# Kernel optimization log

Hardware: AMD Instinct MI355X
Metric: run time of the kernel (lower is better)

Reference implementation:

```python
import jax, jax.numpy as jnp
import numpy as np

B, T, D, H = 4, 2048, 512, 8
DH = D // H

def setup_inputs() -> dict:
    key = jax.random.key(0)
    k1, k2, k3, k4 = jax.random.split(key, 4)
    scale = 1.0 / np.sqrt(D)
    return {
        "x": jax.random.normal(k1, (B, T, D), dtype=jnp.float32),
        "attn_mask": jnp.ones((B, T), dtype=jnp.int32),
        "bias": jax.random.normal(k2, (B, T, T), dtype=jnp.float32),
        "W_qkv": jax.random.normal(k3, (D, 3 * D), dtype=jnp.float32) * scale,
        "W_out": jax.random.normal(k4, (D, D), dtype=jnp.float32) * scale,
    }

def reference(x, attn_mask, bias, W_qkv, W_out):
    qkv = x @ W_qkv                      # [B,T,3D]
    q, k, v = jnp.split(qkv, 3, axis=-1)
    def heads(t):                        # [B,T,D] -> [B,H,T,DH]
        return t.reshape(B, T, H, DH).transpose(0, 2, 1, 3)
    q, k, v = heads(q), heads(k), heads(v)
    logits = jnp.einsum('bhqd,bhkd->bhqk', q, k) / np.sqrt(DH)
    logits = logits + bias[:, None, :, :]
    mask = (attn_mask[:, None, None, :] != 0)
    logits = jnp.where(mask, logits, -jnp.inf)
    attn = jax.nn.softmax(logits, axis=-1)
    out = jnp.einsum('bhqk,bhkd->bhqd', attn, v)  # [B,H,T,DH]
    out = out.transpose(0, 2, 1, 3).reshape(B, T, D)
    return out @ W_out
```

## Files before the change

### kernel.cpp

```cpp
#include <hip/hip_runtime.h>
#include <hip/hip_bf16.h>
#include <stdint.h>

#define Bc 4
#define Tc 2048
#define Dc 512
#define Hc 8

typedef __bf16 bf16x8 __attribute__((ext_vector_type(8)));
typedef float  f32x4  __attribute__((ext_vector_type(4)));
typedef unsigned short u16x8 __attribute__((ext_vector_type(8)));

__device__ __forceinline__ unsigned short f2b(float f) {
  union { float f; unsigned u; } v; v.f = f;
  unsigned r = v.u + 0x7fffu + ((v.u >> 16) & 1u);
  return (unsigned short)(r >> 16);
}

__device__ __forceinline__ bf16x8 ld_frag(const unsigned short* p) {
  u16x8 u = *(const u16x8*)p;
  return __builtin_bit_cast(bf16x8, u);
}

__device__ __forceinline__ void gload_lds16(const unsigned short* g, unsigned short* l) {
  __builtin_amdgcn_global_load_lds((const __attribute__((address_space(1))) void*)g,
                                   (__attribute__((address_space(3))) void*)l,
                                   16, 0, 0);
}

__device__ __forceinline__ unsigned cvtpk_bf16(float lo, float hi) {
  unsigned r;
  asm("v_cvt_pk_bf16_f32 %0, %1, %2" : "=v"(r) : "v"(lo), "v"(hi));
  return r;
}

__global__ __launch_bounds__(256) void cvt_bf16(const float* __restrict__ in,
                                                unsigned short* __restrict__ out, int n) {
  int i = (blockIdx.x * 256 + threadIdx.x) * 8;
  if (i >= n) return;
  float4 a = *(const float4*)&in[i];
  float4 b = *(const float4*)&in[i + 4];
  u16x8 r;
  r[0] = f2b(a.x); r[1] = f2b(a.y); r[2] = f2b(a.z); r[3] = f2b(a.w);
  r[4] = f2b(b.x); r[5] = f2b(b.y); r[6] = f2b(b.z); r[7] = f2b(b.w);
  *(u16x8*)&out[i] = r;
}

__global__ __launch_bounds__(256) void transp_bf16(const float* __restrict__ in,
                                                   unsigned short* __restrict__ out,
                                                   int R, int C) {
  __shared__ float tile[32][33];
  int c0 = blockIdx.x * 32, r0 = blockIdx.y * 32;
  int lx = threadIdx.x & 31, ly = threadIdx.x >> 5;
  #pragma unroll
  for (int i = 0; i < 32; i += 8) tile[ly + i][lx] = in[(size_t)(r0 + ly + i) * C + c0 + lx];
  __syncthreads();
  #pragma unroll
  for (int i = 0; i < 32; i += 8) out[(size_t)(c0 + ly + i) * R + r0 + lx] = f2b(tile[lx][ly + i]);
}

__global__ __launch_bounds__(256) void transp_v(const unsigned short* __restrict__ qkv,
                                                unsigned short* __restrict__ vtg) {
  __shared__ unsigned short tile[32][34];
  int t0 = blockIdx.x * 32;
  int d0 = blockIdx.y * 32;
  int b  = blockIdx.z;
  int lx = threadIdx.x & 31, ly = threadIdx.x >> 5;
  #pragma unroll
  for (int i = 0; i < 32; i += 8)
    tile[ly + i][lx] = qkv[(size_t)(b * Tc + t0 + ly + i) * 1536 + 1024 + d0 + lx];
  __syncthreads();
  #pragma unroll
  for (int i = 0; i < 32; i += 8)
    vtg[(size_t)(b * 512 + d0 + ly + i) * Tc + t0 + lx] = tile[lx][ly + i];
}

template <int N, int OUTF32>
__global__ __launch_bounds__(256) void gemm_bt(const unsigned short* __restrict__ A,
                                               const unsigned short* __restrict__ Bt,
                                               void* __restrict__ Cout, int M, int K) {
  __shared__ unsigned short As[128 * 32];
  __shared__ unsigned short Bs[128 * 32];
  const int tid = threadIdx.x;
  const int lane = tid & 63;
  const int wid = tid >> 6;
  const int wm = (wid >> 1) * 64;
  const int wn = (wid & 1) * 64;
  const int m0 = blockIdx.x * 128;
  const int n0 = blockIdx.y * 128;
  const int l15 = lane & 15;
  const int lg = lane >> 4;

  f32x4 acc[4][4];
  #pragma unroll
  for (int i = 0; i < 4; i++)
    #pragma unroll
    for (int j = 0; j < 4; j++) acc[i][j] = (f32x4){0.f, 0.f, 0.f, 0.f};

  const int srow = tid >> 2;
  const int scol = (tid & 3) * 8;

  for (int k0 = 0; k0 < K; k0 += 32) {
    __syncthreads();
    gload_lds16(&A[(size_t)(m0 + srow) * K + k0 + scol],      &As[tid * 8]);
    gload_lds16(&A[(size_t)(m0 + 64 + srow) * K + k0 + scol], &As[2048 + tid * 8]);
    gload_lds16(&Bt[(size_t)(n0 + srow) * K + k0 + scol],      &Bs[tid * 8]);
    gload_lds16(&Bt[(size_t)(n0 + 64 + srow) * K + k0 + scol], &Bs[2048 + tid * 8]);
    __syncthreads();
    bf16x8 af[4], bfr[4];
    #pragma unroll
    for (int m = 0; m < 4; m++) af[m] = ld_frag(&As[(wm + m * 16 + l15) * 32 + lg * 8]);
    #pragma unroll
    for (int n = 0; n < 4; n++) bfr[n] = ld_frag(&Bs[(wn + n * 16 + l15) * 32 + lg * 8]);
    #pragma unroll
    for (int m = 0; m < 4; m++)
      #pragma unroll
      for (int n = 0; n < 4; n++)
        acc[m][n] = __builtin_amdgcn_mfma_f32_16x16x32_bf16(af[m], bfr[n], acc[m][n], 0, 0, 0);
  }

  #pragma unroll
  for (int m = 0; m < 4; m++)
    #pragma unroll
    for (int n = 0; n < 4; n++)
      #pragma unroll
      for (int j = 0; j < 4; j++) {
        int row = m0 + wm + m * 16 + lg * 4 + j;
        int col = n0 + wn + n * 16 + l15;
        float v = acc[m][n][j];
        if (OUTF32) ((float*)Cout)[(size_t)row * N + col] = v;
        else ((unsigned short*)Cout)[(size_t)row * N + col] = f2b(v);
      }
}

__global__ __launch_bounds__(256) void attn_kernel(const unsigned short* __restrict__ qkv,
                                                   const unsigned short* __restrict__ vtg,
                                                   const float* __restrict__ bias,
                                                   const int* __restrict__ amask,
                                                   unsigned short* __restrict__ ctx) {
  __shared__ unsigned short Ks[64 * 64];
  __shared__ unsigned short Vs[64 * 64];
  __shared__ unsigned short Pt[4][16 * 64];

  const int NQ = Tc / 64;
  const int bid = blockIdx.x;
  const int b = bid / (Hc * NQ);
  const int h = (bid / NQ) % Hc;
  const int q0 = (bid % NQ) * 64;
  const int tid = threadIdx.x;
  const int lane = tid & 63;
  const int w = tid >> 6;
  const int l15 = lane & 15;
  const int lg = lane >> 4;

  const float LOG2E = 1.44269504f;
  const float SC = 0.125f * LOG2E;

  const int qrow = q0 + w * 16 + l15;
  const size_t qoff = (size_t)(b * Tc + qrow) * 1536 + h * 64;
  bf16x8 qf0 = ld_frag(&qkv[qoff + lg * 8]);
  bf16x8 qf1 = ld_frag(&qkv[qoff + 32 + lg * 8]);

  u16x8 ou;
  #pragma unroll
  for (int e = 0; e < 8; e++) ou[e] = 0x3f80;
  const bf16x8 ones = __builtin_bit_cast(bf16x8, ou);

  f32x4 o[4];
  f32x4 osum = (f32x4){0.f, 0.f, 0.f, 0.f};
  #pragma unroll
  for (int n = 0; n < 4; n++) o[n] = (f32x4){0.f, 0.f, 0.f, 0.f};

  const int skey = tid >> 3;
  const int sc = tid & 7;
  const int sgc = sc ^ (skey & 7);

  const size_t kcol = (size_t)b * Tc * 1536 + 512 + h * 64;
  const unsigned short* vrow = &vtg[(size_t)(b * 512 + h * 64) * Tc];

  const float* bq = bias + (size_t)(b * Tc + q0 + w * 16 + l15) * Tc;
  const int* mq = amask + b * Tc;

  unsigned short* ptw = &Pt[w][0];

  for (int kt = 0; kt < Tc; kt += 64) {
    __syncthreads();
    {
      const size_t kbase = kcol + (size_t)kt * 1536;
      gload_lds16(&qkv[kbase + (size_t)skey * 1536 + sgc * 8],        &Ks[tid * 8]);
      gload_lds16(&qkv[kbase + (size_t)(skey + 32) * 1536 + sgc * 8], &Ks[2048 + tid * 8]);
      gload_lds16(&vrow[(size_t)skey * Tc + kt + sgc * 8],        &Vs[tid * 8]);
      gload_lds16(&vrow[(size_t)(skey + 32) * Tc + kt + sgc * 8], &Vs[2048 + tid * 8]);
    }
    float bf_[4][4];
    #pragma unroll
    for (int t2 = 0; t2 < 4; t2++) {
      float4 bb = *(const float4*)&bq[kt + t2 * 16 + lg * 4];
      int4 mm = *(const int4*)&mq[kt + t2 * 16 + lg * 4];
      bf_[t2][0] = mm.x ? bb.x * LOG2E : -1e30f;
      bf_[t2][1] = mm.y ? bb.y * LOG2E : -1e30f;
      bf_[t2][2] = mm.z ? bb.z * LOG2E : -1e30f;
      bf_[t2][3] = mm.w ? bb.w * LOG2E : -1e30f;
    }
    __syncthreads();

    f32x4 s[4];
    __builtin_amdgcn_s_setprio(1);
    #pragma unroll
    for (int t2 = 0; t2 < 4; t2++) {
      int key = t2 * 16 + l15;
      bf16x8 kb0 = ld_frag(&Ks[key * 64 + ((lg) ^ (key & 7)) * 8]);
      bf16x8 kb1 = ld_frag(&Ks[key * 64 + ((4 + lg) ^ (key & 7)) * 8]);
      f32x4 z = (f32x4){0.f, 0.f, 0.f, 0.f};
      z = __builtin_amdgcn_mfma_f32_16x16x32_bf16(kb0, qf0, z, 0, 0, 0);
      z = __builtin_amdgcn_mfma_f32_16x16x32_bf16(kb1, qf1, z, 0, 0, 0);
      s[t2] = z;
    }
    __builtin_amdgcn_s_setprio(0);

    #pragma unroll
    for (int t2 = 0; t2 < 4; t2++) {
      #pragma unroll
      for (int j = 0; j < 4; j++)
        s[t2][j] = exp2f(fmaf(s[t2][j], SC, bf_[t2][j]));
      uint2 pw;
      pw.x = cvtpk_bf16(s[t2][0], s[t2][1]);
      pw.y = cvtpk_bf16(s[t2][2], s[t2][3]);
      const int cp = (2 * t2 + (lg >> 1)) ^ (l15 & 7);
      *(uint2*)&ptw[l15 * 64 + cp * 8 + (lg & 1) * 4] = pw;
    }

    __builtin_amdgcn_s_setprio(1);
    #pragma unroll
    for (int ks = 0; ks < 2; ks++) {
      bf16x8 pa = ld_frag(&ptw[l15 * 64 + ((ks * 4 + lg) ^ (l15 & 7)) * 8]);
      osum = __builtin_amdgcn_mfma_f32_16x16x32_bf16(pa, ones, osum, 0, 0, 0);
      #pragma unroll
      for (int n = 0; n < 4; n++) {
        int d = n * 16 + l15;
        bf16x8 vb = ld_frag(&Vs[d * 64 + ((ks * 4 + lg) ^ (d & 7)) * 8]);
        o[n] = __builtin_amdgcn_mfma_f32_16x16x32_bf16(pa, vb, o[n], 0, 0, 0);
      }
    }
    __builtin_amdgcn_s_setprio(0);
  }

  #pragma unroll
  for (int n = 0; n < 4; n++)
    #pragma unroll
    for (int j = 0; j < 4; j++) {
      int q = q0 + w * 16 + lg * 4 + j;
      ctx[(size_t)(b * Tc + q) * Dc + h * 64 + n * 16 + l15] = f2b(o[n][j] / osum[j]);
    }
}

extern "C" void kernel_launch(void* const* d_in, const int* in_sizes, int n_in,
                              void* d_out, int out_size, void* d_ws, size_t ws_size,
                              hipStream_t stream) {
  const float* x     = (const float*)d_in[0];
  const int*   amask = (const int*)d_in[1];
  const float* bias  = (const float*)d_in[2];
  const float* Wqkv  = (const float*)d_in[3];
  const float* Wout  = (const float*)d_in[4];
  float* out = (float*)d_out;
  char* ws = (char*)d_ws;

  unsigned short* xb    = (unsigned short*)(ws + 0);
  unsigned short* wqkvT = (unsigned short*)(ws + 8388608);
  unsigned short* woutT = (unsigned short*)(ws + 9961472);
  unsigned short* qkv   = (unsigned short*)(ws + 10485760);
  unsigned short* ctx   = (unsigned short*)(ws + 35651584);
  unsigned short* vtg   = (unsigned short*)(ws + 44040192);

  cvt_bf16<<<2048, 256, 0, stream>>>(x, xb, Bc * Tc * Dc);
  transp_bf16<<<dim3(48, 16), 256, 0, stream>>>(Wqkv, wqkvT, 512, 1536);
  transp_bf16<<<dim3(16, 16), 256, 0, stream>>>(Wout, woutT, 512, 512);
  gemm_bt<1536, 0><<<dim3(64, 12), 256, 0, stream>>>(xb, wqkvT, (void*)qkv, 8192, 512);
  transp_v<<<dim3(64, 16, 4), 256, 0, stream>>>(qkv, vtg);
  attn_kernel<<<1024, 256, 0, stream>>>(qkv, vtg, bias, amask, ctx);
  gemm_bt<512, 1><<<dim3(64, 4), 256, 0, stream>>>(ctx, woutT, (void*)out, 8192, 512);
}
```

Measured before the change: 167.4 us.

## Halve attention block to 32 query rows and precompute additive float mask

The attention kernel now runs with 2 waves (32 query rows) per block and 2048 blocks instead of 4 waves and 1024 blocks, so each block's K/V tile loads are spread over 128 threads in four passes. A small pre-kernel converts the int attention mask into an additive float vector (0 or -1e30), and the bias computation becomes a single fma instead of a select. This raises block count and occupancy granularity but doubles K/V tile loading per query row, increasing L2/global traffic for K and V.

```diff
diff --git a/kernel.cpp b/kernel.cpp
--- a/kernel.cpp
+++ b/kernel.cpp
@@ -44,6 +44,12 @@
   r[0] = f2b(a.x); r[1] = f2b(a.y); r[2] = f2b(a.z); r[3] = f2b(a.w);
   r[4] = f2b(b.x); r[5] = f2b(b.y); r[6] = f2b(b.z); r[7] = f2b(b.w);
   *(u16x8*)&out[i] = r;
+}
+
+__global__ __launch_bounds__(256) void mask_f32(const int* __restrict__ amask,
+                                                float* __restrict__ maddv, int n) {
+  int i = blockIdx.x * 256 + threadIdx.x;
+  if (i < n) maddv[i] = amask[i] ? 0.f : -1e30f;
 }
 
 __global__ __launch_bounds__(256) void transp_bf16(const float* __restrict__ in,
@@ -133,20 +139,20 @@
       }
 }
 
-__global__ __launch_bounds__(256) void attn_kernel(const unsigned short* __restrict__ qkv,
+__global__ __launch_bounds__(128) void attn_kernel(const unsigned short* __restrict__ qkv,
                                                    const unsigned short* __restrict__ vtg,
                                                    const float* __restrict__ bias,
-                                                   const int* __restrict__ amask,
+                                                   const float* __restrict__ maddv,
                                                    unsigned short* __restrict__ ctx) {
   __shared__ unsigned short Ks[64 * 64];
   __shared__ unsigned short Vs[64 * 64];
-  __shared__ unsigned short Pt[4][16 * 64];
-
-  const int NQ = Tc / 64;
+  __shared__ unsigned short Pt[2][16 * 64];
+
+  const int NQ = Tc / 32;
   const int bid = blockIdx.x;
   const int b = bid / (Hc * NQ);
   const int h = (bid / NQ) % Hc;
-  const int q0 = (bid % NQ) * 64;
+  const int q0 = (bid % NQ) * 32;
   const int tid = threadIdx.x;
   const int lane = tid & 63;
   const int w = tid >> 6;
@@ -179,7 +185,7 @@
   const unsigned short* vrow = &vtg[(size_t)(b * 512 + h * 64) * Tc];
 
   const float* bq = bias + (size_t)(b * Tc + q0 + w * 16 + l15) * Tc;
-  const int* mq = amask + b * Tc;
+  const float* mf = maddv + b * Tc;
 
   unsigned short* ptw = &Pt[w][0];
 
@@ -187,20 +193,21 @@
     __syncthreads();
     {
       const size_t kbase = kcol + (size_t)kt * 1536;
-      gload_lds16(&qkv[kbase + (size_t)skey * 1536 + sgc * 8],        &Ks[tid * 8]);
-      gload_lds16(&qkv[kbase + (size_t)(skey + 32) * 1536 + sgc * 8], &Ks[2048 + tid * 8]);
-      gload_lds16(&vrow[(size_t)skey * Tc + kt + sgc * 8],        &Vs[tid * 8]);
-      gload_lds16(&vrow[(size_t)(skey + 32) * Tc + kt + sgc * 8], &Vs[2048 + tid * 8]);
+      #pragma unroll
+      for (int i = 0; i < 4; i++) {
+        gload_lds16(&qkv[kbase + (size_t)(skey + 16 * i) * 1536 + sgc * 8], &Ks[i * 1024 + tid * 8]);
+        gload_lds16(&vrow[(size_t)(skey + 16 * i) * Tc + kt + sgc * 8],     &Vs[i * 1024 + tid * 8]);
+      }
     }
     float bf_[4][4];
     #pragma unroll
     for (int t2 = 0; t2 < 4; t2++) {
       float4 bb = *(const float4*)&bq[kt + t2 * 16 + lg * 4];
-      int4 mm = *(const int4*)&mq[kt + t2 * 16 + lg * 4];
-      bf_[t2][0] = mm.x ? bb.x * LOG2E : -1e30f;
-      bf_[t2][1] = mm.y ? bb.y * LOG2E : -1e30f;
-      bf_[t2][2] = mm.z ? bb.z * LOG2E : -1e30f;
-      bf_[t2][3] = mm.w ? bb.w * LOG2E : -1e30f;
+      float4 mm = *(const float4*)&mf[kt + t2 * 16 + lg * 4];
+      bf_[t2][0] = fmaf(bb.x, LOG2E, mm.x);
+      bf_[t2][1] = fmaf(bb.y, LOG2E, mm.y);
+      bf_[t2][2] = fmaf(bb.z, LOG2E, mm.z);
+      bf_[t2][3] = fmaf(bb.w, LOG2E, mm.w);
     }
     __syncthreads();
 
@@ -271,12 +278,14 @@
   unsigned short* qkv   = (unsigned short*)(ws + 10485760);
   unsigned short* ctx   = (unsigned short*)(ws + 35651584);
   unsigned short* vtg   = (unsigned short*)(ws + 44040192);
+  float*          maddv = (float*)(ws + 52428800);
 
   cvt_bf16<<<2048, 256, 0, stream>>>(x, xb, Bc * Tc * Dc);
+  mask_f32<<<32, 256, 0, stream>>>(amask, maddv, Bc * Tc);
   transp_bf16<<<dim3(48, 16), 256, 0, stream>>>(Wqkv, wqkvT, 512, 1536);
   transp_bf16<<<dim3(16, 16), 256, 0, stream>>>(Wout, woutT, 512, 512);
   gemm_bt<1536, 0><<<dim3(64, 12), 256, 0, stream>>>(xb, wqkvT, (void*)qkv, 8192, 512);
   transp_v<<<dim3(64, 16, 4), 256, 0, stream>>>(qkv, vtg);
-  attn_kernel<<<1024, 256, 0, stream>>>(qkv, vtg, bias, amask, ctx);
+  attn_kernel<<<2048, 128, 0, stream>>>(qkv, vtg, bias, maddv, ctx);
   gemm_bt<512, 1><<<dim3(64, 4), 256, 0, stream>>>(ctx, woutT, (void*)out, 8192, 512);
 }
```

After: 176.5 us. 5.5% more time.
